# Kernel optimization log

Measured on AMD Instinct MI355X. Metric: run time of the kernel, lower is better.

Reference implementation:

```python
import jax, jax.numpy as jnp
import numpy as np

N = 4096           # batch size (square similarity matrix)
NUM_BINS = 10      # histogram bins (module default)
NUM_CLASSES = 64   # classes used to synthesize the relevance matrix


def setup_inputs() -> dict:
    key = jax.random.key(0)
    k1, k2 = jax.random.split(key)
    # cosine similarities in [-1, 1]
    batch = jax.random.uniform(k1, (N, N), jnp.float32, -1.0, 1.0)
    # relevance matrix from class labels: labels[i,j] = 1 if same class
    cls = jax.random.randint(k2, (N,), 0, NUM_CLASSES)
    labels = (cls[:, None] == cls[None, :]).astype(jnp.float32)
    return {"batch": batch, "labels": labels}


def reference(batch, labels):
    num_bins = NUM_BINS
    I_pos = labels
    I_neg = 1.0 - labels
    N_pos = jnp.sum(labels, axis=1)                      # [N]
    dist2 = 2.0 - 2.0 * jnp.clip(batch, -1.0, 1.0)       # [N, N], in [0, 4]
    Delta = 4.0 / num_bins
    Z = jnp.linspace(0.0, 4.0, num_bins + 1)             # [L], L = num_bins+1

    # soft binning pulse for all bins at once: [N, N, L]
    pulse = jnp.maximum(0.0, 1.0 - jnp.abs(dist2[..., None] - Z) / Delta)
    h_pos = jnp.einsum('nml,nm->nl', pulse, I_pos)       # [N, L]
    h_neg = jnp.einsum('nml,nm->nl', pulse, I_neg)       # [N, L]

    H_pos = jnp.cumsum(h_pos, axis=1)
    H = jnp.cumsum(h_pos + h_neg, axis=1)

    # FastAP = h_pos * H_pos / H, with nan/inf (H == 0) set to 0
    safe_H = jnp.where(H > 0, H, 1.0)
    ap_terms = jnp.where(H > 0, h_pos * H_pos / safe_H, 0.0)

    safe_Np = jnp.where(N_pos > 0, N_pos, 1.0)
    ap = jnp.sum(ap_terms, axis=1) / safe_Np             # [N]

    # drop NaN rows (N_pos == 0) from the mean, matching FastAP[~isnan]
    valid = N_pos > 0
    mean_ap = jnp.sum(jnp.where(valid, ap, 0.0)) / jnp.sum(valid.astype(ap.dtype))
    return 1.0 - mean_ap
```

## Files before the change

### kernel.cpp

```cpp
#include <hip/hip_runtime.h>

#define N 4096
#define NUM_BINS 10
#define L (NUM_BINS + 1)
#define BLOCK 256
#define WAVES_PER_BLOCK (BLOCK / 64)
#define F4_PER_ROW (N / 4)
#define ITERS (F4_PER_ROW / 64)

__global__ __launch_bounds__(BLOCK) void fastap_row_kernel(
    const float* __restrict__ batch, const float* __restrict__ labels,
    float* __restrict__ ap_out, float* __restrict__ valid_out)
{
    const int lane = threadIdx.x & 63;
    const int wave = threadIdx.x >> 6;
    const int row  = blockIdx.x * WAVES_PER_BLOCK + wave;

    const float4* b4 = (const float4*)(batch  + (size_t)row * N);
    const float4* l4 = (const float4*)(labels + (size_t)row * N);

    float acc_pos[L];
    float acc_all[L];
    #pragma unroll
    for (int l = 0; l < L; ++l) { acc_pos[l] = 0.f; acc_all[l] = 0.f; }

    #pragma unroll 4
    for (int it = 0; it < ITERS; ++it) {
        float4 bv = b4[it * 64 + lane];
        float4 lv = l4[it * 64 + lane];
        #pragma unroll
        for (int e = 0; e < 4; ++e) {
            float x   = ((const float*)&bv)[e];
            float lbl = ((const float*)&lv)[e];
            x = fminf(fmaxf(x, -1.f), 1.f);
            float t = fmaf(-5.f, x, 5.f);
            #pragma unroll
            for (int l = 0; l < L; ++l) {
                float p = fmaxf(0.f, 1.f - fabsf(t - (float)l));
                acc_pos[l] = fmaf(p, lbl, acc_pos[l]);
                acc_all[l] += p;
            }
        }
    }

    #pragma unroll
    for (int l = 0; l < L; ++l) {
        #pragma unroll
        for (int off = 1; off < 64; off <<= 1) {
            acc_pos[l] += __shfl_xor(acc_pos[l], off, 64);
            acc_all[l] += __shfl_xor(acc_all[l], off, 64);
        }
    }

    if (lane == 0) {
        float Hp = 0.f, Hs = 0.f, ap = 0.f;
        #pragma unroll
        for (int l = 0; l < L; ++l) {
            float hp = acc_pos[l];
            Hp += hp;
            Hs += acc_all[l];
            if (Hs > 0.f) ap += hp * Hp / Hs;
        }
        float Np = Hp;
        ap_out[row]    = (Np > 0.f) ? ap / Np : 0.f;
        valid_out[row] = (Np > 0.f) ? 1.f : 0.f;
    }
}

__global__ __launch_bounds__(BLOCK) void fastap_reduce_kernel(
    const float* __restrict__ ap, const float* __restrict__ valid,
    float* __restrict__ out)
{
    const int tid = threadIdx.x;
    float s_ap = 0.f, s_v = 0.f;
    for (int i = tid; i < N; i += BLOCK) {
        s_ap += ap[i];
        s_v  += valid[i];
    }
    #pragma unroll
    for (int off = 32; off > 0; off >>= 1) {
        s_ap += __shfl_down(s_ap, off, 64);
        s_v  += __shfl_down(s_v,  off, 64);
    }
    __shared__ float r_ap[BLOCK / 64], r_v[BLOCK / 64];
    const int wave = tid >> 6;
    if ((tid & 63) == 0) { r_ap[wave] = s_ap; r_v[wave] = s_v; }
    __syncthreads();
    if (tid == 0) {
        float ta = 0.f, tv = 0.f;
        #pragma unroll
        for (int w = 0; w < BLOCK / 64; ++w) { ta += r_ap[w]; tv += r_v[w]; }
        out[0] = 1.f - ta / tv;
    }
}

extern "C" void kernel_launch(void* const* d_in, const int* in_sizes, int n_in,
                              void* d_out, int out_size, void* d_ws, size_t ws_size,
                              hipStream_t stream) {
    const float* batch  = (const float*)d_in[0];
    const float* labels = (const float*)d_in[1];
    float* ap    = (float*)d_ws;
    float* valid = ap + N;
    fastap_row_kernel<<<N / WAVES_PER_BLOCK, BLOCK, 0, stream>>>(batch, labels, ap, valid);
    fastap_reduce_kernel<<<1, BLOCK, 0, stream>>>(ap, valid, (float*)d_out);
}
```

Baseline: 152.8 us.

## Assign one block per row, preload row into registers, atomically accumulate AP

Each row is now handled by a whole 256-thread block instead of a single wave. All four float4 loads per thread for both matrices are issued up front, then the per-wave histograms are combined through shared memory. The per-row AP and valid count are added into two global accumulators with atomics, so the second reduction kernel becomes a one-thread finalize preceded by a memset. This aims to expose more memory-level parallelism per row, at the cost of a block-wide sync, contended float atomics whose summation order is nondeterministic, and an extra memset launch.

Measured after the change: 223.2 us. 46.1% more time.

```diff
diff --git a/kernel.cpp b/kernel.cpp
--- a/kernel.cpp
+++ b/kernel.cpp
@@ -4,34 +4,37 @@
 #define NUM_BINS 10
 #define L (NUM_BINS + 1)
 #define BLOCK 256
-#define WAVES_PER_BLOCK (BLOCK / 64)
-#define F4_PER_ROW (N / 4)
-#define ITERS (F4_PER_ROW / 64)
+#define WPB (BLOCK / 64)
+#define F4T (N / 4 / BLOCK)
 
 __global__ __launch_bounds__(BLOCK) void fastap_row_kernel(
     const float* __restrict__ batch, const float* __restrict__ labels,
-    float* __restrict__ ap_out, float* __restrict__ valid_out)
+    float* __restrict__ accum)
 {
-    const int lane = threadIdx.x & 63;
-    const int wave = threadIdx.x >> 6;
-    const int row  = blockIdx.x * WAVES_PER_BLOCK + wave;
+    const int tid  = threadIdx.x;
+    const int lane = tid & 63;
+    const int wave = tid >> 6;
+    const int row  = blockIdx.x;
 
     const float4* b4 = (const float4*)(batch  + (size_t)row * N);
     const float4* l4 = (const float4*)(labels + (size_t)row * N);
 
-    float acc_pos[L];
-    float acc_all[L];
+    float4 bv[F4T], lv[F4T];
+    #pragma unroll
+    for (int i = 0; i < F4T; ++i) bv[i] = b4[i * BLOCK + tid];
+    #pragma unroll
+    for (int i = 0; i < F4T; ++i) lv[i] = l4[i * BLOCK + tid];
+
+    float acc_pos[L], acc_all[L];
     #pragma unroll
     for (int l = 0; l < L; ++l) { acc_pos[l] = 0.f; acc_all[l] = 0.f; }
 
-    #pragma unroll 4
-    for (int it = 0; it < ITERS; ++it) {
-        float4 bv = b4[it * 64 + lane];
-        float4 lv = l4[it * 64 + lane];
+    #pragma unroll
+    for (int i = 0; i < F4T; ++i) {
         #pragma unroll
         for (int e = 0; e < 4; ++e) {
-            float x   = ((const float*)&bv)[e];
-            float lbl = ((const float*)&lv)[e];
+            float x   = ((const float*)&bv[i])[e];
+            float lbl = ((const float*)&lv[i])[e];
             x = fminf(fmaxf(x, -1.f), 1.f);
             float t = fmaf(-5.f, x, 5.f);
             #pragma unroll
@@ -52,46 +55,39 @@
         }
     }
 
+    __shared__ float s_pos[WPB][L], s_all[WPB][L];
     if (lane == 0) {
+        #pragma unroll
+        for (int l = 0; l < L; ++l) {
+            s_pos[wave][l] = acc_pos[l];
+            s_all[wave][l] = acc_all[l];
+        }
+    }
+    __syncthreads();
+
+    if (tid == 0) {
         float Hp = 0.f, Hs = 0.f, ap = 0.f;
         #pragma unroll
         for (int l = 0; l < L; ++l) {
-            float hp = acc_pos[l];
+            float hp = 0.f, ha = 0.f;
+            #pragma unroll
+            for (int w = 0; w < WPB; ++w) { hp += s_pos[w][l]; ha += s_all[w][l]; }
             Hp += hp;
-            Hs += acc_all[l];
+            Hs += ha;
             if (Hs > 0.f) ap += hp * Hp / Hs;
         }
         float Np = Hp;
-        ap_out[row]    = (Np > 0.f) ? ap / Np : 0.f;
-        valid_out[row] = (Np > 0.f) ? 1.f : 0.f;
+        if (Np > 0.f) {
+            atomicAdd(&accum[0], ap / Np);
+            atomicAdd(&accum[1], 1.f);
+        }
     }
 }
 
-__global__ __launch_bounds__(BLOCK) void fastap_reduce_kernel(
-    const float* __restrict__ ap, const float* __restrict__ valid,
-    float* __restrict__ out)
+__global__ void fastap_finalize(const float* __restrict__ accum,
+                                float* __restrict__ out)
 {
-    const int tid = threadIdx.x;
-    float s_ap = 0.f, s_v = 0.f;
-    for (int i = tid; i < N; i += BLOCK) {
-        s_ap += ap[i];
-        s_v  += valid[i];
-    }
-    #pragma unroll
-    for (int off = 32; off > 0; off >>= 1) {
-        s_ap += __shfl_down(s_ap, off, 64);
-        s_v  += __shfl_down(s_v,  off, 64);
-    }
-    __shared__ float r_ap[BLOCK / 64], r_v[BLOCK / 64];
-    const int wave = tid >> 6;
-    if ((tid & 63) == 0) { r_ap[wave] = s_ap; r_v[wave] = s_v; }
-    __syncthreads();
-    if (tid == 0) {
-        float ta = 0.f, tv = 0.f;
-        #pragma unroll
-        for (int w = 0; w < BLOCK / 64; ++w) { ta += r_ap[w]; tv += r_v[w]; }
-        out[0] = 1.f - ta / tv;
-    }
+    out[0] = 1.f - accum[0] / accum[1];
 }
 
 extern "C" void kernel_launch(void* const* d_in, const int* in_sizes, int n_in,
@@ -99,8 +95,8 @@
                               hipStream_t stream) {
     const float* batch  = (const float*)d_in[0];
     const float* labels = (const float*)d_in[1];
-    float* ap    = (float*)d_ws;
-    float* valid = ap + N;
-    fastap_row_kernel<<<N / WAVES_PER_BLOCK, BLOCK, 0, stream>>>(batch, labels, ap, valid);
-    fastap_reduce_kernel<<<1, BLOCK, 0, stream>>>(ap, valid, (float*)d_out);
+    float* accum = (float*)d_ws;
+    hipMemsetAsync(accum, 0, 2 * sizeof(float), stream);
+    fastap_row_kernel<<<N, BLOCK, 0, stream>>>(batch, labels, accum);
+    fastap_finalize<<<1, 1, 0, stream>>>(accum, (float*)d_out);
 }
```

## Compute cumulative histogram directly via clamped ramps and split rows across two waves

Applied to the files above, without the earlier changes.

Replaces per-bin triangular pulse accumulation with cumulative clamped-ramp sums, so the cumulative histogram is computed directly with fewer ALU ops per bin and one fewer bin; the last bin is recovered from the positive count and N. Each row is split across two waves, which combine partial sums through shared memory. This aims to reduce the ALU-bound inner loop cost and raise parallelism, at the cost of a block sync and reliance on the total count equalling N.

Result: slower. 171.3 us (+12.1%).

```diff
diff --git a/kernel.cpp b/kernel.cpp
--- a/kernel.cpp
+++ b/kernel.cpp
@@ -1,67 +1,84 @@
 #include <hip/hip_runtime.h>
 
 #define N 4096
-#define NUM_BINS 10
-#define L (NUM_BINS + 1)
+#define NBINS 10
 #define BLOCK 256
-#define WAVES_PER_BLOCK (BLOCK / 64)
-#define F4_PER_ROW (N / 4)
-#define ITERS (F4_PER_ROW / 64)
+#define ROWS_PER_BLOCK 2
+#define HALF (N / 2)
+#define F4_PER_LANE (HALF / 4 / 64)
 
-__global__ __launch_bounds__(BLOCK) void fastap_row_kernel(
+__global__ __launch_bounds__(BLOCK, 8) void fastap_row_kernel(
     const float* __restrict__ batch, const float* __restrict__ labels,
     float* __restrict__ ap_out, float* __restrict__ valid_out)
 {
-    const int lane = threadIdx.x & 63;
-    const int wave = threadIdx.x >> 6;
-    const int row  = blockIdx.x * WAVES_PER_BLOCK + wave;
+    const int tid  = threadIdx.x;
+    const int lane = tid & 63;
+    const int wave = tid >> 6;
+    const int rsub = wave >> 1;
+    const int half = wave & 1;
+    const int row  = blockIdx.x * ROWS_PER_BLOCK + rsub;
 
-    const float4* b4 = (const float4*)(batch  + (size_t)row * N);
-    const float4* l4 = (const float4*)(labels + (size_t)row * N);
+    const float4* b4 = (const float4*)(batch  + (size_t)row * N + half * HALF);
+    const float4* l4 = (const float4*)(labels + (size_t)row * N + half * HALF);
 
-    float acc_pos[L];
-    float acc_all[L];
+    float hc_pos[NBINS], hc_all[NBINS], np = 0.f;
     #pragma unroll
-    for (int l = 0; l < L; ++l) { acc_pos[l] = 0.f; acc_all[l] = 0.f; }
+    for (int l = 0; l < NBINS; ++l) { hc_pos[l] = 0.f; hc_all[l] = 0.f; }
 
-    #pragma unroll 4
-    for (int it = 0; it < ITERS; ++it) {
+    #pragma unroll 2
+    for (int it = 0; it < F4_PER_LANE; ++it) {
         float4 bv = b4[it * 64 + lane];
         float4 lv = l4[it * 64 + lane];
         #pragma unroll
         for (int e = 0; e < 4; ++e) {
             float x   = ((const float*)&bv)[e];
             float lbl = ((const float*)&lv)[e];
-            x = fminf(fmaxf(x, -1.f), 1.f);
-            float t = fmaf(-5.f, x, 5.f);
+            float u = fmaf(5.f, x, -4.f);
+            np += lbl;
             #pragma unroll
-            for (int l = 0; l < L; ++l) {
-                float p = fmaxf(0.f, 1.f - fabsf(t - (float)l));
-                acc_pos[l] = fmaf(p, lbl, acc_pos[l]);
-                acc_all[l] += p;
+            for (int l = 0; l < NBINS; ++l) {
+                float c = u + (float)l;
+                c = fminf(fmaxf(c, 0.f), 1.f);
+                hc_pos[l] = fmaf(c, lbl, hc_pos[l]);
+                hc_all[l] += c;
             }
         }
     }
 
     #pragma unroll
-    for (int l = 0; l < L; ++l) {
+    for (int off = 1; off < 64; off <<= 1) {
         #pragma unroll
-        for (int off = 1; off < 64; off <<= 1) {
-            acc_pos[l] += __shfl_xor(acc_pos[l], off, 64);
-            acc_all[l] += __shfl_xor(acc_all[l], off, 64);
+        for (int l = 0; l < NBINS; ++l) {
+            hc_pos[l] += __shfl_xor(hc_pos[l], off, 64);
+            hc_all[l] += __shfl_xor(hc_all[l], off, 64);
         }
+        np += __shfl_xor(np, off, 64);
     }
 
+    __shared__ float s[4][2 * NBINS + 1];
     if (lane == 0) {
-        float Hp = 0.f, Hs = 0.f, ap = 0.f;
         #pragma unroll
-        for (int l = 0; l < L; ++l) {
-            float hp = acc_pos[l];
-            Hp += hp;
-            Hs += acc_all[l];
-            if (Hs > 0.f) ap += hp * Hp / Hs;
+        for (int l = 0; l < NBINS; ++l) {
+            s[wave][l]         = hc_pos[l];
+            s[wave][NBINS + l] = hc_all[l];
         }
-        float Np = Hp;
+        s[wave][2 * NBINS] = np;
+    }
+    __syncthreads();
+
+    if (lane == 0 && half == 0) {
+        const int w0 = rsub * 2, w1 = w0 + 1;
+        float Hp_prev = 0.f, ap = 0.f;
+        #pragma unroll
+        for (int l = 0; l < NBINS; ++l) {
+            float Hp = s[w0][l] + s[w1][l];
+            float Ha = s[w0][NBINS + l] + s[w1][NBINS + l];
+            float hp = Hp - Hp_prev;
+            if (Ha > 0.f) ap += hp * Hp / Ha;
+            Hp_prev = Hp;
+        }
+        float Np = s[w0][2 * NBINS] + s[w1][2 * NBINS];
+        ap += (Np - Hp_prev) * Np * (1.f / (float)N);
         ap_out[row]    = (Np > 0.f) ? ap / Np : 0.f;
         valid_out[row] = (Np > 0.f) ? 1.f : 0.f;
     }
@@ -101,6 +118,6 @@
     const float* labels = (const float*)d_in[1];
     float* ap    = (float*)d_ws;
     float* valid = ap + N;
-    fastap_row_kernel<<<N / WAVES_PER_BLOCK, BLOCK, 0, stream>>>(batch, labels, ap, valid);
+    fastap_row_kernel<<<N / ROWS_PER_BLOCK, BLOCK, 0, stream>>>(batch, labels, ap, valid);
     fastap_reduce_kernel<<<1, BLOCK, 0, stream>>>(ap, valid, (float*)d_out);
 }
```
